# Optimization experiments

Hardware: AMD Instinct MI355X
Metric: run time of the kernel (lower is better)

Reference implementation:

```python
import jax, jax.numpy as jnp
import numpy as np

# Config (mirrors init_kwargs)
B, S = 1, 2048          # batch, seq_len
H = 2048                # hidden_size
NH, NKV = 16, 8         # attention heads, kv heads (GQA n_rep = 2)
HD = H // NH            # head_dim = 128
I = 5632                # intermediate_size
L = 2                   # num_hidden_layers
V = 32000               # vocab_size
WIN = 1024              # sliding_window
THETA = 10000.0
EPS = 1e-6


def setup_inputs() -> dict:
    key = jax.random.key(0)
    ks = jax.random.split(key, 12)
    s = 0.02
    return {
        "input_ids": jax.random.randint(ks[0], (B, S), 0, V, dtype=jnp.int32),
        "embed": jax.random.normal(ks[1], (V, H), jnp.float32) * s,
        "Wq": jax.random.normal(ks[2], (L, H, NH * HD), jnp.float32) * s,
        "Wk": jax.random.normal(ks[3], (L, H, NKV * HD), jnp.float32) * s,
        "Wv": jax.random.normal(ks[4], (L, H, NKV * HD), jnp.float32) * s,
        "Wo": jax.random.normal(ks[5], (L, NH * HD, H), jnp.float32) * s,
        "Wg": jax.random.normal(ks[6], (L, H, I), jnp.float32) * s,
        "Wu": jax.random.normal(ks[7], (L, H, I), jnp.float32) * s,
        "Wd": jax.random.normal(ks[8], (L, I, H), jnp.float32) * s,
        "ln1": jnp.ones((L, H), jnp.float32),
        "ln2": jnp.ones((L, H), jnp.float32),
        "norm_w": jnp.ones((H,), jnp.float32),
    }


def _rmsnorm(x, w, eps=EPS):
    return x * jax.lax.rsqrt(jnp.mean(x * x, axis=-1, keepdims=True) + eps) * w


def _rope_tables(seq_len, dim, theta):
    inv_freq = 1.0 / (theta ** (jnp.arange(0, dim, 2, dtype=jnp.float32) / dim))
    freqs = jnp.arange(seq_len, dtype=jnp.float32)[:, None] * inv_freq[None, :]  # [S, dim/2]
    emb = jnp.concatenate([freqs, freqs], axis=-1)  # [S, dim]
    return jnp.cos(emb), jnp.sin(emb)


def _rotate_half(x):
    half = x.shape[-1] // 2
    return jnp.concatenate([-x[..., half:], x[..., :half]], axis=-1)


def _sliding_window_causal_mask(seq_len, window, dtype):
    i = jnp.arange(seq_len)[:, None]
    j = jnp.arange(seq_len)[None, :]
    allowed = (j <= i) & (j >= i - window)  # band: causal + sliding window
    return jnp.where(allowed, 0.0, jnp.finfo(dtype).min).astype(dtype)[None, None]  # [1,1,S,S]


def _forward(input_ids, embed, Wq, Wk, Wv, Wo, Wg, Wu, Wd, ln1, ln2, norm_w):
    x = embed[input_ids]  # [B,S,H]
    cos, sin = _rope_tables(S, HD, THETA)          # [S,HD]
    cos = cos[None, :, None, :]                    # [1,S,1,HD]
    sin = sin[None, :, None, :]
    mask = _sliding_window_causal_mask(S, WIN, x.dtype)  # [1,1,S,S]
    scale = 1.0 / jnp.sqrt(jnp.float32(HD)).astype(x.dtype)
    n_rep = NH // NKV

    for l in range(L):
        # --- attention block ---
        h = _rmsnorm(x, ln1[l])
        q = (h @ Wq[l]).reshape(B, S, NH, HD)
        k = (h @ Wk[l]).reshape(B, S, NKV, HD)
        v = (h @ Wv[l]).reshape(B, S, NKV, HD)
        q = q * cos + _rotate_half(q) * sin
        k = k * cos + _rotate_half(k) * sin
        # repeat_kv (GQA)
        k = jnp.broadcast_to(k[:, :, :, None, :], (B, S, NKV, n_rep, HD)).reshape(B, S, NH, HD)
        v = jnp.broadcast_to(v[:, :, :, None, :], (B, S, NKV, n_rep, HD)).reshape(B, S, NH, HD)
        scores = jnp.einsum('bshn,bthn->bhst', q, k) * scale + mask  # [B,NH,S,S]
        attn = jax.nn.softmax(scores.astype(jnp.float32), axis=-1).astype(x.dtype)
        o = jnp.einsum('bhst,bthn->bshn', attn, v).reshape(B, S, NH * HD)
        x = x + o @ Wo[l]
        # --- MLP block (SwiGLU) ---
        h = _rmsnorm(x, ln2[l])
        x = x + (jax.nn.silu(h @ Wg[l]) * (h @ Wu[l])) @ Wd[l]

    return _rmsnorm(x, norm_w)


def reference(input_ids, embed, Wq, Wk, Wv, Wo, Wg, Wu, Wd, ln1, ln2, norm_w):
    return _forward(input_ids, embed, Wq, Wk, Wv, Wo, Wg, Wu, Wd, ln1, ln2, norm_w)
```

## Files before the change

### kernel.cpp

```cpp
#include <hip/hip_runtime.h>
#include <stdint.h>

using bf16x8 = __attribute__((ext_vector_type(8))) __bf16;
using f32x4  = __attribute__((ext_vector_type(4))) float;

#define DEVI __device__ __forceinline__

DEVI unsigned short f2b(float f) {
  unsigned int u = __builtin_bit_cast(unsigned int, f);
  u = (u + 0x7FFFu + ((u >> 16) & 1u)) >> 16;
  return (unsigned short)u;
}
DEVI float b2f(unsigned short h) {
  unsigned int u = ((unsigned int)h) << 16;
  return __builtin_bit_cast(float, u);
}
DEVI f32x4 mfma16(bf16x8 a, bf16x8 b, f32x4 c) {
  return __builtin_amdgcn_mfma_f32_16x16x32_bf16(a, b, c, 0, 0, 0);
}
#define GLD(gp, lp) __builtin_amdgcn_global_load_lds( \
    (__attribute__((address_space(1))) void*)(uintptr_t)(gp), \
    (__attribute__((address_space(3))) void*)(uintptr_t)(lp), 16, 0, 0)

static constexpr int S_LEN = 2048;
static constexpr int HDIM  = 2048;
static constexpr int NH    = 16;
static constexpr int NKV   = 8;
static constexpr int HD    = 128;
static constexpr int IFF   = 5632;
static constexpr int WIN   = 1024;

__global__ __launch_bounds__(256) void gather_kernel(const int* __restrict__ ids,
    const float* __restrict__ embed, float* __restrict__ x,
    float* __restrict__ ct, float* __restrict__ st) {
  int s = blockIdx.x, t = threadIdx.x;
  const float4* src = (const float4*)(embed + (size_t)ids[s] * HDIM);
  float4* dst = (float4*)(x + (size_t)s * HDIM);
  dst[t]       = src[t];
  dst[t + 256] = src[t + 256];
  if (t < 64) {
    float inv = expf(-(float)t * (9.210340371976184f / 64.0f));
    float f = (float)s * inv;
    ct[s * 64 + t] = cosf(f);
    st[s * 64 + t] = sinf(f);
  }
}

DEVI void rms_finish(float4 v0, float4 v1, const float* __restrict__ w,
                     void* __restrict__ outp, int s, int t, int outf32) {
  float ss = v0.x*v0.x + v0.y*v0.y + v0.z*v0.z + v0.w*v0.w +
             v1.x*v1.x + v1.y*v1.y + v1.z*v1.z + v1.w*v1.w;
  #pragma unroll
  for (int off = 32; off >= 1; off >>= 1) ss += __shfl_xor(ss, off, 64);
  __shared__ float red[4];
  if ((t & 63) == 0) red[t >> 6] = ss;
  __syncthreads();
  ss = red[0] + red[1] + red[2] + red[3];
  float rr = rsqrtf(ss * (1.0f / 2048.0f) + 1e-6f);
  const float4* w4 = (const float4*)w;
  float4 w0 = w4[t], w1 = w4[t + 256];
  float o0x = v0.x*rr*w0.x, o0y = v0.y*rr*w0.y, o0z = v0.z*rr*w0.z, o0w = v0.w*rr*w0.w;
  float o1x = v1.x*rr*w1.x, o1y = v1.y*rr*w1.y, o1z = v1.z*rr*w1.z, o1w = v1.w*rr*w1.w;
  if (outf32) {
    float4* o4 = (float4*)outp + (size_t)s * 512;
    o4[t]       = make_float4(o0x, o0y, o0z, o0w);
    o4[t + 256] = make_float4(o1x, o1y, o1z, o1w);
  } else {
    uint2* ob = (uint2*)((unsigned short*)outp + (size_t)s * HDIM);
    ob[t]       = make_uint2((unsigned)f2b(o0x) | ((unsigned)f2b(o0y) << 16),
                             (unsigned)f2b(o0z) | ((unsigned)f2b(o0w) << 16));
    ob[t + 256] = make_uint2((unsigned)f2b(o1x) | ((unsigned)f2b(o1y) << 16),
                             (unsigned)f2b(o1z) | ((unsigned)f2b(o1w) << 16));
  }
}

__global__ __launch_bounds__(256) void rmsnorm_kernel(const float* __restrict__ x,
    const float* __restrict__ w, void* __restrict__ outp) {
  int s = blockIdx.x, t = threadIdx.x;
  const float4* row = (const float4*)(x + (size_t)s * HDIM);
  rms_finish(row[t], row[t + 256], w, outp, s, t, 0);
}

template<int OUTF32, int NPARTS>
__global__ __launch_bounds__(256) void rmsnorm_combine_kernel(
    float* __restrict__ x, const float* __restrict__ parts,
    const float* __restrict__ w, void* __restrict__ outp) {
  int s = blockIdx.x, t = threadIdx.x;
  const size_t PS = (size_t)2048 * 2048;
  float4* row = (float4*)(x + (size_t)s * HDIM);
  float4 v0 = row[t], v1 = row[t + 256];
  #pragma unroll
  for (int p = 0; p < NPARTS; ++p) {
    const float4* pr = (const float4*)(parts + p * PS + (size_t)s * HDIM);
    float4 a = pr[t], b = pr[t + 256];
    v0.x += a.x; v0.y += a.y; v0.z += a.z; v0.w += a.w;
    v1.x += b.x; v1.y += b.y; v1.z += b.z; v1.w += b.w;
  }
  row[t] = v0; row[t + 256] = v1;
  rms_finish(v0, v1, w, outp, s, t, OUTF32);
}

__global__ __launch_bounds__(256) void posttrans_kernel(const float* __restrict__ qkvf,
    const float* __restrict__ ct, const float* __restrict__ st,
    unsigned short* __restrict__ qo, unsigned short* __restrict__ ko,
    unsigned short* __restrict__ vt) {
  __shared__ float tl[64 * 65];
  int b = blockIdx.x;
  if (b < 2048) {
    int s = b, t = threadIdx.x;
    #pragma unroll
    for (int it = 0; it < 6; ++it) {
      int idx = it * 256 + t;
      int head = idx >> 6, d = idx & 63;
      float c = ct[s * 64 + d], sn = st[s * 64 + d];
      if (head < NH) {
        const float* base = qkvf + (size_t)s * 4096 + head * HD;
        float a = base[d], bb = base[d + 64];
        unsigned short* dst = qo + (size_t)s * (NH * HD) + head * HD;
        dst[d]      = f2b(a * c - bb * sn);
        dst[d + 64] = f2b(bb * c + a * sn);
      } else {
        int kh = head - NH;
        const float* base = qkvf + (size_t)s * 4096 + 2048 + kh * HD;
        float a = base[d], bb = base[d + 64];
        unsigned short* dst = ko + (size_t)s * (NKV * HD) + kh * HD;
        dst[d]      = f2b(a * c - bb * sn);
        dst[d + 64] = f2b(bb * c + a * sn);
      }
    }
  } else {
    int t = b - 2048;
    int k0 = (t / 16) * 64, n0 = (t % 16) * 64;
    int tx = threadIdx.x & 63, ty = threadIdx.x >> 6;
    const float* in = qkvf + 3072;
    #pragma unroll
    for (int i = 0; i < 16; ++i)
      tl[(ty + 4 * i) * 65 + tx] = in[(size_t)(k0 + ty + 4 * i) * 4096 + (n0 + tx)];
    __syncthreads();
    #pragma unroll
    for (int i = 0; i < 16; ++i)
      vt[(size_t)(n0 + ty + 4 * i) * 2048 + (k0 + tx)] = f2b(tl[tx * 65 + (ty + 4 * i)]);
  }
}

DEVI void tile_transpose_cvt(const float* __restrict__ in, int istr,
    unsigned short* __restrict__ out, int ostr, int k0, int n0, int ob, float* tl) {
  int tx = threadIdx.x & 63, ty = threadIdx.x >> 6;
  #pragma unroll
  for (int i = 0; i < 16; ++i)
    tl[(ty + 4 * i) * 65 + tx] = in[(size_t)(k0 + ty + 4 * i) * istr + (n0 + tx)];
  __syncthreads();
  #pragma unroll
  for (int i = 0; i < 16; ++i)
    out[(size_t)(ob + ty + 4 * i) * ostr + (k0 + tx)] = f2b(tl[tx * 65 + (ty + 4 * i)]);
}

__global__ __launch_bounds__(256) void convert_weights_kernel(
    const float* __restrict__ Wq, const float* __restrict__ Wk,
    const float* __restrict__ Wv, const float* __restrict__ Wo,
    const float* __restrict__ Wg, const float* __restrict__ Wu,
    const float* __restrict__ Wd,
    unsigned short* wqkvT, unsigned short* woT,
    unsigned short* wguT, unsigned short* wdT) {
  __shared__ float tl[64 * 65];
  int b = blockIdx.x;
  const float* in; unsigned short* out; int istr, ostr, tilesN, t; int guAdd = -1;
  if (b < 1024)      { in = Wq; out = wqkvT;                       istr = 2048; ostr = 2048; tilesN = 32; t = b; }
  else if (b < 1536) { in = Wk; out = wqkvT + (size_t)2048 * 2048; istr = 1024; ostr = 2048; tilesN = 16; t = b - 1024; }
  else if (b < 2048) { in = Wv; out = wqkvT + (size_t)3072 * 2048; istr = 1024; ostr = 2048; tilesN = 16; t = b - 1536; }
  else if (b < 3072) { in = Wo; out = woT;                         istr = 2048; ostr = 2048; tilesN = 32; t = b - 2048; }
  else if (b < 5888) { in = Wg; out = wguT;                        istr = 5632; ostr = 2048; tilesN = 88; t = b - 3072; guAdd = 0; }
  else if (b < 8704) { in = Wu; out = wguT;                        istr = 5632; ostr = 2048; tilesN = 88; t = b - 5888; guAdd = 128; }
  else               { in = Wd; out = wdT;                         istr = 2048; ostr = 5632; tilesN = 32; t = b - 8704; }
  int k0 = (t / tilesN) * 64, n0 = (t % tilesN) * 64;
  int ob = (guAdd >= 0) ? (((n0 >> 7) << 8) + (n0 & 64) + guAdd) : n0;
  tile_transpose_cvt(in, istr, out, ostr, k0, n0, ob, tl);
}

DEVI bf16x8 ldsAB(const unsigned short* buf, int r, int cbyte) {
  return *(const bf16x8*)((const unsigned char*)buf + r * 128 + (cbyte ^ ((r & 7) << 4)));
}
DEVI void stage_unit(const unsigned short* __restrict__ G, int Kstr,
                     unsigned short* lbuf, int loff0, int grow0,
                     int loff1, int grow1, int w, int l) {
  const int rsub = l >> 3;
  const int ce = ((l & 7) ^ rsub) << 3;
  const unsigned short* s0 = G + (size_t)(grow0 + w * 8 + rsub) * Kstr + ce;
  GLD(s0, (unsigned char*)lbuf + loff0 + w * 1024 + l * 16);
  const unsigned short* s1 = G + (size_t)(grow1 + w * 8 + rsub) * Kstr + ce;
  GLD(s1, (unsigned char*)lbuf + loff1 + w * 1024 + l * 16);
}
template<int Q>
DEVI void phase128(const unsigned short* Ab, f32x4 (&acc)[4][4],
                   bf16x8 (&breg)[2][4], int wr, int lg, int li) {
  const int r0 = wr * 64 + Q * 16 + li;
  bf16x8 a0 = ldsAB(Ab, r0, lg * 16);
  bf16x8 a1 = ldsAB(Ab, r0, 64 + lg * 16);
  __builtin_amdgcn_s_setprio(1);
  #pragma unroll
  for (int n = 0; n < 4; ++n) acc[Q][n] = mfma16(a0, breg[0][n], acc[Q][n]);
  #pragma unroll
  for (int n = 0; n < 4; ++n) acc[Q][n] = mfma16(a1, breg[1][n], acc[Q][n]);
  __builtin_amdgcn_s_setprio(0);
}

template<int EPI>
__global__ __launch_bounds__(512, 1) void gemm128_kernel(
    const unsigned short* __restrict__ A, const unsigned short* __restrict__ Bt,
    void* __restrict__ Cout, int Kstr, int nt, int parts, int nbm, int ldc,
    long long partStride) {
  __shared__ __align__(16) unsigned char smem[98304];
  unsigned short* As0 = (unsigned short*)smem;
  unsigned short* Bs0 = (unsigned short*)(smem + 32768);
  const int tid = threadIdx.x, l = tid & 63, w = tid >> 6;
  const int lg = l >> 4, li = l & 15;
  const int wr = w >> 2, wc = w & 3;
  const int nb = gridDim.x, qx = nb >> 3;
  const int wg = ((int)blockIdx.x & 7) * qx + ((int)blockIdx.x >> 3);
  const int nbT = nb / parts;
  const int tile = wg % nbT, part = wg / nbT;
  const int m0 = (tile % nbm) * 128, n0 = (tile / nbm) * 256;
  const int kOff = part * (nt << 6);
  const unsigned short* At  = A  + (size_t)m0 * Kstr + kOff;
  const unsigned short* Bto = Bt + (size_t)n0 * Kstr + kOff;
  f32x4 acc[4][4] = {};
  bf16x8 breg[2][4];

  stage_unit(Bto, Kstr, Bs0, 0, 0, 8192, 64, w, l);
  stage_unit(Bto, Kstr, Bs0, 16384, 128, 24576, 192, w, l);
  stage_unit(At,  Kstr, As0, 0, 0, 8192, 64, w, l);
  { int k1 = (nt > 1) ? 64 : 0;
    stage_unit(Bto + k1, Kstr, Bs0 + 16384, 0, 0, 8192, 64, w, l);
    stage_unit(Bto + k1, Kstr, Bs0 + 16384, 16384, 128, 24576, 192, w, l); }
  asm volatile("s_waitcnt vmcnt(4)\n\ts_barrier" ::: "memory");

  for (int t = 0; t < nt; ++t) {
    unsigned short* Ab  = As0 + (t & 1) * 8192;
    unsigned short* Bb  = Bs0 + (t & 1) * 16384;
    unsigned short* Abn = As0 + ((t & 1) ^ 1) * 8192;
    const int kt1 = ((t + 1 < nt) ? t + 1 : nt - 1) << 6;
    const int kt2 = ((t + 2 < nt) ? t + 2 : nt - 1) << 6;
    stage_unit(At + kt1, Kstr, Abn, 0, 0, 8192, 64, w, l);
    #pragma unroll
    for (int ks = 0; ks < 2; ++ks)
      #pragma unroll
      for (int n = 0; n < 4; ++n)
        breg[ks][n] = ldsAB(Bb, wc * 64 + n * 16 + li, ks * 64 + lg * 16);
    asm volatile("s_waitcnt lgkmcnt(0)\n\ts_barrier" ::: "memory");
    phase128<0>(Ab, acc, breg, wr, lg, li);
    stage_unit(Bto + kt2, Kstr, Bb, 0, 0, 8192, 64, w, l);
    phase128<1>(Ab, acc, breg, wr, lg, li);
    stage_unit(Bto + kt2, Kstr, Bb, 16384, 128, 24576, 192, w, l);
    phase128<2>(Ab, acc, breg, wr, lg, li);
    phase128<3>(Ab, acc, breg, wr, lg, li);
    asm volatile("s_waitcnt vmcnt(4) lgkmcnt(0)\n\ts_barrier" ::: "memory");
  }
  asm volatile("s_waitcnt vmcnt(0)" ::: "memory");

  if (EPI == 0) {
    float* C = (float*)Cout + (size_t)part * (size_t)partStride;
    #pragma unroll
    for (int m = 0; m < 4; ++m)
      #pragma unroll
      for (int n = 0; n < 4; ++n) {
        int col = n0 + wc * 64 + n * 16 + li;
        #pragma unroll
        for (int r = 0; r < 4; ++r) {
          int row = m0 + wr * 64 + m * 16 + lg * 4 + r;
          C[(size_t)row * ldc + col] = acc[m][n][r];
        }
      }
  } else {
    float* ub = (float*)smem;
    asm volatile("s_barrier" ::: "memory");
    if (wc >= 2) {
      #pragma unroll
      for (int m = 0; m < 4; ++m)
        #pragma unroll
        for (int n = 0; n < 4; ++n) {
          int colL = (wc - 2) * 64 + n * 16 + li;
          #pragma unroll
          for (int r = 0; r < 4; ++r) {
            int rowl = wr * 64 + m * 16 + lg * 4 + r;
            ub[rowl * 128 + colL] = acc[m][n][r];
          }
        }
    }
    asm volatile("s_waitcnt lgkmcnt(0)\n\ts_barrier" ::: "memory");
    if (wc < 2) {
      unsigned short* act = (unsigned short*)Cout;
      const int col0 = n0 >> 1;
      #pragma unroll
      for (int m = 0; m < 4; ++m)
        #pragma unroll
        for (int n = 0; n < 4; ++n) {
          int colL = wc * 64 + n * 16 + li;
          #pragma unroll
          for (int r = 0; r < 4; ++r) {
            int rowl = wr * 64 + m * 16 + lg * 4 + r;
            float g = acc[m][n][r];
            float u = ub[rowl * 128 + colL];
            act[(size_t)(m0 + rowl) * ldc + col0 + colL] =
                f2b(g / (1.0f + __expf(-g)) * u);
          }
        }
    }
  }
}

DEVI void stageKV(const unsigned short* __restrict__ kg,
                  const unsigned short* __restrict__ vtg, int kv, int j0,
                  unsigned short* Kbuf, unsigned short* Vbuf, int w, int l) {
  #pragma unroll
  for (int p = 0; p < 2; ++p) {
    int off = p * 8192 + w * 1024 + l * 16;
    int row = off >> 8;
    int colb = (off & 255) ^ ((row & 7) << 4);
    GLD(kg + (size_t)(j0 + row) * (NKV * HD) + kv * HD + (colb >> 1),
        (unsigned char*)Kbuf + off);
  }
  #pragma unroll
  for (int p = 0; p < 2; ++p) {
    int off = p * 8192 + w * 1024 + l * 16;
    int d = off >> 7;
    int colb = (off & 127) ^ ((d & 7) << 4);
    GLD(vtg + (size_t)(kv * HD + d) * S_LEN + j0 + (colb >> 1),
        (unsigned char*)Vbuf + off);
  }
}

__global__ __launch_bounds__(512) void attn_kernel(
    const unsigned short* __restrict__ qg, const unsigned short* __restrict__ kg,
    const unsigned short* __restrict__ vtg, unsigned short* __restrict__ og) {
  __shared__ __align__(16) unsigned short Kl[2][64 * 128];
  __shared__ __align__(16) unsigned short Vtl[2][128 * 64];
  __shared__ __align__(16) unsigned short Plds[8][16 * 72];
  const int tid = threadIdx.x, l = tid & 63, w = tid >> 6;
  const int lg = l >> 4, li = l & 15;
  const int i0 = blockIdx.x * 64, kv = blockIdx.y;
  const int hq = kv * 2 + (w >> 2);
  const int qr0 = i0 + (w & 3) * 16;
  const float scale = 0.08838834764831845f;

  bf16x8 qf[4];
  {
    const unsigned short* qrow = qg + (size_t)(qr0 + li) * (NH * HD) + hq * HD;
    #pragma unroll
    for (int sl = 0; sl < 4; ++sl)
      qf[sl] = *(const bf16x8*)(qrow + sl * 32 + lg * 8);
  }
  f32x4 oacc[8] = {};
  float mrow[4] = {-1e30f, -1e30f, -1e30f, -1e30f};
  float srow[4] = {0.f, 0.f, 0.f, 0.f};

  int jstart = i0 - WIN; if (jstart < 0) jstart = 0;
  stageKV(kg, vtg, kv, jstart, Kl[0], Vtl[0], w, l);

  int it = 0;
  for (int j0 = jstart; j0 <= i0; j0 += 64, ++it) {
    const int cur = it & 1;
    asm volatile("s_waitcnt vmcnt(0) lgkmcnt(0)\n\ts_barrier" ::: "memory");
    if (j0 + 64 <= i0)
      stageKV(kg, vtg, kv, j0 + 64, Kl[cur ^ 1], Vtl[cur ^ 1], w, l);
    const unsigned short* Klds  = Kl[cur];
    const unsigned short* Vtlds = Vtl[cur];

    f32x4 sacc[4] = {};
    #pragma unroll
    for (int nt = 0; nt < 4; ++nt) {
      int kr = nt * 16 + li;
      #pragma unroll
      for (int sl = 0; sl < 4; ++sl) {
        int cb = (sl * 64 + lg * 16) ^ ((kr & 7) << 4);
        bf16x8 kf = *(const bf16x8*)&Klds[(kr * 256 + cb) >> 1];
        sacc[nt] = mfma16(qf[sl], kf, sacc[nt]);
      }
    }

    float pv[4][4];
    #pragma unroll
    for (int r = 0; r < 4; ++r) {
      int qi = qr0 + lg * 4 + r;
      float sval[4];
      float tm = -1e30f;
      #pragma unroll
      for (int nt = 0; nt < 4; ++nt) {
        int j = j0 + nt * 16 + li;
        bool ok = (j <= qi) && (j + WIN >= qi);
        float sv = ok ? sacc[nt][r] * scale : -1e30f;
        sval[nt] = sv;
        tm = fmaxf(tm, sv);
      }
      #pragma unroll
      for (int off2 = 1; off2 < 16; off2 <<= 1)
        tm = fmaxf(tm, __shfl_xor(tm, off2, 64));
      float mnew = fmaxf(mrow[r], tm);
      float resc = __expf(mrow[r] - mnew);
      mrow[r] = mnew;
      float rs = 0.f;
      #pragma unroll
      for (int nt = 0; nt < 4; ++nt) {
        float p = (sval[nt] > -9e29f) ? __expf(sval[nt] - mnew) : 0.f;
        pv[nt][r] = p;
        rs += p;
      }
      #pragma unroll
      for (int off2 = 1; off2 < 16; off2 <<= 1)
        rs += __shfl_xor(rs, off2, 64);
      srow[r] = srow[r] * resc + rs;
      #pragma unroll
      for (int dt = 0; dt < 8; ++dt) oacc[dt][r] *= resc;
    }

    #pragma unroll
    for (int r = 0; r < 4; ++r)
      #pragma unroll
      for (int nt = 0; nt < 4; ++nt)
        Plds[w][(lg * 4 + r) * 72 + nt * 16 + li] = f2b(pv[nt][r]);
    bf16x8 ap[2];
    #pragma unroll
    for (int ks = 0; ks < 2; ++ks)
      ap[ks] = *(const bf16x8*)&Plds[w][li * 72 + ks * 32 + lg * 8];
    #pragma unroll
    for (int dt = 0; dt < 8; ++dt) {
      int d = dt * 16 + li;
      #pragma unroll
      for (int ks = 0; ks < 2; ++ks) {
        int cb = (ks * 64 + lg * 16) ^ ((d & 7) << 4);
        bf16x8 vf = *(const bf16x8*)&Vtlds[(d * 128 + cb) >> 1];
        oacc[dt] = mfma16(ap[ks], vf, oacc[dt]);
      }
    }
  }

  #pragma unroll
  for (int r = 0; r < 4; ++r) {
    float inv = 1.0f / srow[r];
    int qi = qr0 + lg * 4 + r;
    unsigned short* orow = og + (size_t)qi * (NH * HD) + hq * HD;
    #pragma unroll
    for (int dt = 0; dt < 8; ++dt)
      orow[dt * 16 + li] = f2b(oacc[dt][r] * inv);
  }
}

extern "C" void kernel_launch(void* const* d_in, const int* in_sizes, int n_in,
                              void* d_out, int out_size, void* d_ws, size_t ws_size,
                              hipStream_t stream) {
  const int*   ids   = (const int*)d_in[0];
  const float* embed = (const float*)d_in[1];
  const float* Wq    = (const float*)d_in[2];
  const float* Wk    = (const float*)d_in[3];
  const float* Wv    = (const float*)d_in[4];
  const float* Wo    = (const float*)d_in[5];
  const float* Wg    = (const float*)d_in[6];
  const float* Wu    = (const float*)d_in[7];
  const float* Wd    = (const float*)d_in[8];
  const float* ln1   = (const float*)d_in[9];
  const float* ln2   = (const float*)d_in[10];
  const float* normw = (const float*)d_in[11];

  uint8_t* ws = (uint8_t*)d_ws;
  unsigned short* wqkvT = (unsigned short*)(ws + 0);
  unsigned short* woT   = (unsigned short*)(ws + 16777216ull);
  unsigned short* wguT  = (unsigned short*)(ws + 25165824ull);
  unsigned short* wdT   = (unsigned short*)(ws + 71303168ull);
  float*          x     = (float*)(ws + 94371840ull);
  unsigned short* h     = (unsigned short*)(ws + 111149056ull);
  unsigned short* q     = (unsigned short*)(ws + 119537664ull);
  unsigned short* k     = (unsigned short*)(ws + 127926272ull);
  unsigned short* vt    = (unsigned short*)(ws + 132120576ull);
  unsigned short* o     = (unsigned short*)(ws + 136314880ull);
  unsigned short* act   = (unsigned short*)(ws + 119537664ull);
  float*          pbuf  = (float*)(ws + 144703488ull);
  float*          cost  = (float*)(ws + 213909504ull);
  float*          sint  = (float*)(ws + 214433792ull);
  const long long PSo = 4194304LL;

  gather_kernel<<<2048, 256, 0, stream>>>(ids, embed, x, cost, sint);

  for (int l = 0; l < 2; ++l) {
    convert_weights_kernel<<<11520, 256, 0, stream>>>(
        Wq + (size_t)l * 2048 * 2048, Wk + (size_t)l * 2048 * 1024,
        Wv + (size_t)l * 2048 * 1024, Wo + (size_t)l * 2048 * 2048,
        Wg + (size_t)l * 2048 * 5632, Wu + (size_t)l * 2048 * 5632,
        Wd + (size_t)l * 5632 * 2048,
        wqkvT, woT, wguT, wdT);
    if (l == 0)
      rmsnorm_kernel<<<2048, 256, 0, stream>>>(x, ln1, h);
    else
      rmsnorm_combine_kernel<0, 2><<<2048, 256, 0, stream>>>(x, pbuf, ln1 + 2048, h);
    gemm128_kernel<0><<<256, 512, 0, stream>>>(h, wqkvT, pbuf, 2048, 32, 1, 16, 4096, 0);
    posttrans_kernel<<<2560, 256, 0, stream>>>(pbuf, cost, sint, q, k, vt);
    attn_kernel<<<dim3(32, 8), 512, 0, stream>>>(q, k, vt, o);
    gemm128_kernel<0><<<256, 512, 0, stream>>>(o, woT, pbuf, 2048, 16, 2, 16, 2048, PSo);
    rmsnorm_combine_kernel<0, 2><<<2048, 256, 0, stream>>>(x, pbuf, ln2 + l * 2048, h);
    gemm128_kernel<3><<<704, 512, 0, stream>>>(h, wguT, act, 2048, 32, 1, 16, 5632, 0);
    gemm128_kernel<0><<<256, 512, 0, stream>>>(act, wdT, pbuf, 5632, 44, 2, 16, 2048, PSo);
  }
  rmsnorm_combine_kernel<1, 2><<<2048, 256, 0, stream>>>(x, pbuf, normw, d_out);
  (void)in_sizes; (void)n_in; (void)out_size; (void)ws_size;
}
```

Baseline: 699.0 us.

## Fuse first RMSNorm into gather, emit bf16 QKV, widen weight-convert tiles

```diff
diff --git a/kernel.cpp b/kernel.cpp
--- a/kernel.cpp
+++ b/kernel.cpp
@@ -29,22 +29,6 @@
 static constexpr int HD    = 128;
 static constexpr int IFF   = 5632;
 static constexpr int WIN   = 1024;
-
-__global__ __launch_bounds__(256) void gather_kernel(const int* __restrict__ ids,
-    const float* __restrict__ embed, float* __restrict__ x,
-    float* __restrict__ ct, float* __restrict__ st) {
-  int s = blockIdx.x, t = threadIdx.x;
-  const float4* src = (const float4*)(embed + (size_t)ids[s] * HDIM);
-  float4* dst = (float4*)(x + (size_t)s * HDIM);
-  dst[t]       = src[t];
-  dst[t + 256] = src[t + 256];
-  if (t < 64) {
-    float inv = expf(-(float)t * (9.210340371976184f / 64.0f));
-    float f = (float)s * inv;
-    ct[s * 64 + t] = cosf(f);
-    st[s * 64 + t] = sinf(f);
-  }
-}
 
 DEVI void rms_finish(float4 v0, float4 v1, const float* __restrict__ w,
                      void* __restrict__ outp, int s, int t, int outf32) {
@@ -74,11 +58,23 @@
   }
 }
 
-__global__ __launch_bounds__(256) void rmsnorm_kernel(const float* __restrict__ x,
-    const float* __restrict__ w, void* __restrict__ outp) {
+__global__ __launch_bounds__(256) void gather_kernel(const int* __restrict__ ids,
+    const float* __restrict__ embed, float* __restrict__ x,
+    float* __restrict__ ct, float* __restrict__ st,
+    const float* __restrict__ ln1w, unsigned short* __restrict__ h) {
   int s = blockIdx.x, t = threadIdx.x;
-  const float4* row = (const float4*)(x + (size_t)s * HDIM);
-  rms_finish(row[t], row[t + 256], w, outp, s, t, 0);
+  const float4* src = (const float4*)(embed + (size_t)ids[s] * HDIM);
+  float4* dst = (float4*)(x + (size_t)s * HDIM);
+  float4 v0 = src[t], v1 = src[t + 256];
+  dst[t]       = v0;
+  dst[t + 256] = v1;
+  if (t < 64) {
+    float inv = expf(-(float)t * (9.210340371976184f / 64.0f));
+    float f = (float)s * inv;
+    ct[s * 64 + t] = cosf(f);
+    st[s * 64 + t] = sinf(f);
+  }
+  rms_finish(v0, v1, ln1w, h, s, t, 0);
 }
 
 template<int OUTF32, int NPARTS>
@@ -100,7 +96,7 @@
   rms_finish(v0, v1, w, outp, s, t, OUTF32);
 }
 
-__global__ __launch_bounds__(256) void posttrans_kernel(const float* __restrict__ qkvf,
+__global__ __launch_bounds__(256) void posttrans_kernel(const unsigned short* __restrict__ qkvb,
     const float* __restrict__ ct, const float* __restrict__ st,
     unsigned short* __restrict__ qo, unsigned short* __restrict__ ko,
     unsigned short* __restrict__ vt) {
@@ -114,15 +110,15 @@
       int head = idx >> 6, d = idx & 63;
       float c = ct[s * 64 + d], sn = st[s * 64 + d];
       if (head < NH) {
-        const float* base = qkvf + (size_t)s * 4096 + head * HD;
-        float a = base[d], bb = base[d + 64];
+        const unsigned short* base = qkvb + (size_t)s * 4096 + head * HD;
+        float a = b2f(base[d]), bb = b2f(base[d + 64]);
         unsigned short* dst = qo + (size_t)s * (NH * HD) + head * HD;
         dst[d]      = f2b(a * c - bb * sn);
         dst[d + 64] = f2b(bb * c + a * sn);
       } else {
         int kh = head - NH;
-        const float* base = qkvf + (size_t)s * 4096 + 2048 + kh * HD;
-        float a = base[d], bb = base[d + 64];
+        const unsigned short* base = qkvb + (size_t)s * 4096 + 2048 + kh * HD;
+        float a = b2f(base[d]), bb = b2f(base[d + 64]);
         unsigned short* dst = ko + (size_t)s * (NKV * HD) + kh * HD;
         dst[d]      = f2b(a * c - bb * sn);
         dst[d + 64] = f2b(bb * c + a * sn);
@@ -132,27 +128,15 @@
     int t = b - 2048;
     int k0 = (t / 16) * 64, n0 = (t % 16) * 64;
     int tx = threadIdx.x & 63, ty = threadIdx.x >> 6;
-    const float* in = qkvf + 3072;
+    const unsigned short* in = qkvb + 3072;
     #pragma unroll
     for (int i = 0; i < 16; ++i)
-      tl[(ty + 4 * i) * 65 + tx] = in[(size_t)(k0 + ty + 4 * i) * 4096 + (n0 + tx)];
+      tl[(ty + 4 * i) * 65 + tx] = b2f(in[(size_t)(k0 + ty + 4 * i) * 4096 + (n0 + tx)]);
     __syncthreads();
     #pragma unroll
     for (int i = 0; i < 16; ++i)
       vt[(size_t)(n0 + ty + 4 * i) * 2048 + (k0 + tx)] = f2b(tl[tx * 65 + (ty + 4 * i)]);
   }
-}
-
-DEVI void tile_transpose_cvt(const float* __restrict__ in, int istr,
-    unsigned short* __restrict__ out, int ostr, int k0, int n0, int ob, float* tl) {
-  int tx = threadIdx.x & 63, ty = threadIdx.x >> 6;
-  #pragma unroll
-  for (int i = 0; i < 16; ++i)
-    tl[(ty + 4 * i) * 65 + tx] = in[(size_t)(k0 + ty + 4 * i) * istr + (n0 + tx)];
-  __syncthreads();
-  #pragma unroll
-  for (int i = 0; i < 16; ++i)
-    out[(size_t)(ob + ty + 4 * i) * ostr + (k0 + tx)] = f2b(tl[tx * 65 + (ty + 4 * i)]);
 }
 
 __global__ __launch_bounds__(256) void convert_weights_kernel(
@@ -162,19 +146,32 @@
     const float* __restrict__ Wd,
     unsigned short* wqkvT, unsigned short* woT,
     unsigned short* wguT, unsigned short* wdT) {
-  __shared__ float tl[64 * 65];
+  __shared__ float tl[128 * 65];
   int b = blockIdx.x;
   const float* in; unsigned short* out; int istr, ostr, tilesN, t; int guAdd = -1;
-  if (b < 1024)      { in = Wq; out = wqkvT;                       istr = 2048; ostr = 2048; tilesN = 32; t = b; }
-  else if (b < 1536) { in = Wk; out = wqkvT + (size_t)2048 * 2048; istr = 1024; ostr = 2048; tilesN = 16; t = b - 1024; }
-  else if (b < 2048) { in = Wv; out = wqkvT + (size_t)3072 * 2048; istr = 1024; ostr = 2048; tilesN = 16; t = b - 1536; }
-  else if (b < 3072) { in = Wo; out = woT;                         istr = 2048; ostr = 2048; tilesN = 32; t = b - 2048; }
-  else if (b < 5888) { in = Wg; out = wguT;                        istr = 5632; ostr = 2048; tilesN = 88; t = b - 3072; guAdd = 0; }
-  else if (b < 8704) { in = Wu; out = wguT;                        istr = 5632; ostr = 2048; tilesN = 88; t = b - 5888; guAdd = 128; }
-  else               { in = Wd; out = wdT;                         istr = 2048; ostr = 5632; tilesN = 32; t = b - 8704; }
-  int k0 = (t / tilesN) * 64, n0 = (t % tilesN) * 64;
+  if (b < 512)       { in = Wq; out = wqkvT;                       istr = 2048; ostr = 2048; tilesN = 32; t = b; }
+  else if (b < 768)  { in = Wk; out = wqkvT + (size_t)2048 * 2048; istr = 1024; ostr = 2048; tilesN = 16; t = b - 512; }
+  else if (b < 1024) { in = Wv; out = wqkvT + (size_t)3072 * 2048; istr = 1024; ostr = 2048; tilesN = 16; t = b - 768; }
+  else if (b < 1536) { in = Wo; out = woT;                         istr = 2048; ostr = 2048; tilesN = 32; t = b - 1024; }
+  else if (b < 2944) { in = Wg; out = wguT;                        istr = 5632; ostr = 2048; tilesN = 88; t = b - 1536; guAdd = 0; }
+  else if (b < 4352) { in = Wu; out = wguT;                        istr = 5632; ostr = 2048; tilesN = 88; t = b - 2944; guAdd = 128; }
+  else               { in = Wd; out = wdT;                         istr = 2048; ostr = 5632; tilesN = 32; t = b - 4352; }
+  int k0 = (t / tilesN) * 128, n0 = (t % tilesN) * 64;
+  int tx = threadIdx.x & 63, ty = threadIdx.x >> 6;
+  #pragma unroll
+  for (int i = 0; i < 32; ++i)
+    tl[(ty + 4 * i) * 65 + tx] = in[(size_t)(k0 + ty + 4 * i) * istr + (n0 + tx)];
+  __syncthreads();
   int ob = (guAdd >= 0) ? (((n0 >> 7) << 8) + (n0 & 64) + guAdd) : n0;
-  tile_transpose_cvt(in, istr, out, ostr, k0, n0, ob, tl);
+  unsigned int* ou = (unsigned int*)out;
+  const int kstr2 = ostr >> 1;
+  #pragma unroll
+  for (int i = 0; i < 16; ++i) {
+    int nrow = ty + 4 * i;
+    float lo = tl[(2 * tx) * 65 + nrow], hi = tl[(2 * tx + 1) * 65 + nrow];
+    ou[(size_t)(ob + nrow) * kstr2 + (k0 >> 1) + tx] =
+        (unsigned int)f2b(lo) | ((unsigned int)f2b(hi) << 16);
+  }
 }
 
 DEVI bf16x8 ldsAB(const unsigned short* buf, int r, int cbyte) {
@@ -270,6 +267,19 @@
           C[(size_t)row * ldc + col] = acc[m][n][r];
         }
       }
+  } else if (EPI == 1) {
+    unsigned short* C = (unsigned short*)Cout;
+    #pragma unroll
+    for (int m = 0; m < 4; ++m)
+      #pragma unroll
+      for (int n = 0; n < 4; ++n) {
+        int col = n0 + wc * 64 + n * 16 + li;
+        #pragma unroll
+        for (int r = 0; r < 4; ++r) {
+          int row = m0 + wr * 64 + m * 16 + lg * 4 + r;
+          C[(size_t)row * ldc + col] = f2b(acc[m][n][r]);
+        }
+      }
   } else {
     float* ub = (float*)smem;
     asm volatile("s_barrier" ::: "memory");
@@ -473,25 +483,24 @@
   unsigned short* o     = (unsigned short*)(ws + 136314880ull);
   unsigned short* act   = (unsigned short*)(ws + 119537664ull);
   float*          pbuf  = (float*)(ws + 144703488ull);
+  unsigned short* qkvb  = (unsigned short*)(ws + 144703488ull);
   float*          cost  = (float*)(ws + 213909504ull);
   float*          sint  = (float*)(ws + 214433792ull);
   const long long PSo = 4194304LL;
 
-  gather_kernel<<<2048, 256, 0, stream>>>(ids, embed, x, cost, sint);
+  gather_kernel<<<2048, 256, 0, stream>>>(ids, embed, x, cost, sint, ln1, h);
 
   for (int l = 0; l < 2; ++l) {
-    convert_weights_kernel<<<11520, 256, 0, stream>>>(
+    convert_weights_kernel<<<5760, 256, 0, stream>>>(
         Wq + (size_t)l * 2048 * 2048, Wk + (size_t)l * 2048 * 1024,
         Wv + (size_t)l * 2048 * 1024, Wo + (size_t)l * 2048 * 2048,
         Wg + (size_t)l * 2048 * 5632, Wu + (size_t)l * 2048 * 5632,
         Wd + (size_t)l * 5632 * 2048,
         wqkvT, woT, wguT, wdT);
-    if (l == 0)
-      rmsnorm_kernel<<<2048, 256, 0, stream>>>(x, ln1, h);
-    else
+    if (l == 1)
       rmsnorm_combine_kernel<0, 2><<<2048, 256, 0, stream>>>(x, pbuf, ln1 + 2048, h);
-    gemm128_kernel<0><<<256, 512, 0, stream>>>(h, wqkvT, pbuf, 2048, 32, 1, 16, 4096, 0);
-    posttrans_kernel<<<2560, 256, 0, stream>>>(pbuf, cost, sint, q, k, vt);
+    gemm128_kernel<1><<<256, 512, 0, stream>>>(h, wqkvT, qkvb, 2048, 32, 1, 16, 4096, 0);
+    posttrans_kernel<<<2560, 256, 0, stream>>>(qkvb, cost, sint, q, k, vt);
     attn_kernel<<<dim3(32, 8), 512, 0, stream>>>(q, k, vt, o);
     gemm128_kernel<0><<<256, 512, 0, stream>>>(o, woT, pbuf, 2048, 16, 2, 16, 2048, PSo);
     rmsnorm_combine_kernel<0, 2><<<2048, 256, 0, stream>>>(x, pbuf, ln2 + l * 2048, h);
```

After: 691.6 us. Within noise of the previous version (-1.1%).
